# Kernel tuning notes

Hardware: AMD Instinct MI355X
Metric: run time of the kernel (lower is better)

## Reference

```python
import jax, jax.numpy as jnp
import numpy as np

N_NODES = 50000
N_EDGES = 800000
H = 128


def _mlp2(x, W1, b1, W2, b2):
    # Linear -> ReLU -> Linear
    h = jax.nn.relu(x @ W1 + b1)
    return h @ W2 + b2


def setup_inputs() -> dict:
    key = jax.random.key(0)
    ks = jax.random.split(key, 12)
    glorot = lambda k, fi, fo: jax.random.normal(k, (fi, fo), jnp.float32) * (1.0 / np.sqrt(fi))
    return {
        "x": jax.random.normal(ks[0], (N_NODES, H), jnp.float32),
        "edge_index": jax.random.randint(ks[1], (2, N_EDGES), 0, N_NODES, dtype=jnp.int64),
        "edge_attr": jax.random.normal(ks[2], (N_EDGES, H), jnp.float32),
        # edge MLP: 3H -> H -> H
        "We1": glorot(ks[3], 3 * H, H),
        "be1": jnp.zeros((H,), jnp.float32),
        "We2": glorot(ks[4], H, H),
        "be2": jnp.zeros((H,), jnp.float32),
        # node MLP: 2H -> H -> H
        "Wn1": glorot(ks[5], 2 * H, H),
        "bn1": jnp.zeros((H,), jnp.float32),
        "Wn2": glorot(ks[6], H, H),
        "bn2": jnp.zeros((H,), jnp.float32),
    }


def reference(x, edge_index, edge_attr, We1, be1, We2, be2, Wn1, bn1, Wn2, bn2):
    row, col = edge_index[0], edge_index[1]
    # gather + concat -> edge MLP  [E, 3H] -> [E, H]
    edge_inputs = jnp.concatenate([x[row], x[col], edge_attr], axis=-1)
    messages = _mlp2(edge_inputs, We1, be1, We2, be2)
    # scatter_add by destination node
    agg = jax.ops.segment_sum(messages, col, num_segments=x.shape[0])
    # concat -> node MLP  [N, 2H] -> [N, H]
    node_inputs = jnp.concatenate([x, agg], axis=-1)
    return _mlp2(node_inputs, Wn1, bn1, Wn2, bn2)
```

## Files before the change

### kernel.cpp

```cpp
#include <hip/hip_runtime.h>
#include <hip/hip_bf16.h>
#include <stdint.h>

#define N_NODES 50000
#define N_EDGES 800000
#define H 128

typedef short bf16x8 __attribute__((ext_vector_type(8)));
typedef float f32x4 __attribute__((ext_vector_type(4)));

__device__ __forceinline__ short f2bfs(float f) {
    __hip_bfloat16 h = __float2bfloat16(f);
    return *(short*)&h;
}

__device__ __forceinline__ bf16x8 cvt8(const float* __restrict__ p) {
    const float4* q = (const float4*)p;
    float4 a = q[0], b = q[1];
    bf16x8 r;
    r[0] = f2bfs(a.x); r[1] = f2bfs(a.y); r[2] = f2bfs(a.z); r[3] = f2bfs(a.w);
    r[4] = f2bfs(b.x); r[5] = f2bfs(b.y); r[6] = f2bfs(b.z); r[7] = f2bfs(b.w);
    return r;
}

__global__ void prep_weights(const float* __restrict__ We1, const float* __restrict__ We2,
                             const float* __restrict__ Wn1, const float* __restrict__ Wn2,
                             unsigned short* __restrict__ wb) {
    int i = blockIdx.x * 256 + threadIdx.x;
    if (i >= 114688) return;
    const float* W; int idx;
    if (i < 49152)      { W = We1; idx = i; }
    else if (i < 65536) { W = We2; idx = i - 49152; }
    else if (i < 98304) { W = Wn1; idx = i - 65536; }
    else                { W = Wn2; idx = i - 98304; }
    int f = idx >> 9, lane = (idx >> 3) & 63, j = idx & 7;
    int kt = f >> 3, nt = f & 7;
    int k = kt * 32 + (lane >> 4) * 8 + j;
    int n = nt * 16 + (lane & 15);
    wb[i] = (unsigned short)f2bfs(W[k * H + n]);
}

__launch_bounds__(256)
__global__ void edge_mlp(const float* __restrict__ x,
                         const int* __restrict__ ei,
                         const float* __restrict__ ea,
                         const float* __restrict__ be1,
                         const float* __restrict__ be2,
                         const unsigned short* __restrict__ wb,
                         float* __restrict__ agg) {
    __shared__ short hbuf[4][2][4][64][8];
    const int tid = threadIdx.x;
    const int wave = tid >> 6, lane = tid & 63;
    const int c = lane & 15, quad = lane >> 4;
    const int e0 = (blockIdx.x * 4 + wave) * 32;

    const bf16x8* __restrict__ BW1 = (const bf16x8*)wb;
    const bf16x8* __restrict__ BW2 = (const bf16x8*)(wb + 49152);

    float be1v[8], be2v[8];
#pragma unroll
    for (int nt = 0; nt < 8; ++nt) {
        be1v[nt] = be1[nt * 16 + c];
        be2v[nt] = be2[nt * 16 + c];
    }

    const float* pa[2][3];
#pragma unroll
    for (int t = 0; t < 2; ++t) {
        int e = e0 + t * 16 + c;
        int r  = ei[e];
        int cl = ei[N_EDGES + e];
        pa[t][0] = x + (size_t)r * H;
        pa[t][1] = x + (size_t)cl * H;
        pa[t][2] = ea + (size_t)e * H;
    }

    f32x4 acc[2][8];
#pragma unroll
    for (int t = 0; t < 2; ++t)
#pragma unroll
        for (int nt = 0; nt < 8; ++nt)
            acc[t][nt] = (f32x4){be1v[nt], be1v[nt], be1v[nt], be1v[nt]};

#pragma unroll
    for (int kt = 0; kt < 12; ++kt) {
        const int seg = kt >> 2;
        const int off = (kt & 3) * 32 + quad * 8;
        bf16x8 a0 = cvt8(pa[0][seg] + off);
        bf16x8 a1 = cvt8(pa[1][seg] + off);
#pragma unroll
        for (int nt = 0; nt < 8; ++nt) {
            bf16x8 b = BW1[(kt * 8 + nt) * 64 + lane];
            acc[0][nt] = __builtin_amdgcn_mfma_f32_16x16x32_bf16(a0, b, acc[0][nt], 0, 0, 0);
            acc[1][nt] = __builtin_amdgcn_mfma_f32_16x16x32_bf16(a1, b, acc[1][nt], 0, 0, 0);
        }
    }

#pragma unroll
    for (int t = 0; t < 2; ++t)
#pragma unroll
        for (int nt = 0; nt < 8; ++nt) {
            int kt2 = nt >> 1;
            int laneq = 16 * ((nt * 2 + (c >> 3)) & 3);
#pragma unroll
            for (int r = 0; r < 4; ++r) {
                float v = acc[t][nt][r];
                v = v > 0.f ? v : 0.f;
                hbuf[wave][t][kt2][quad * 4 + r + laneq][c & 7] = f2bfs(v);
            }
        }
    __syncthreads();

    f32x4 acc2[2][8];
#pragma unroll
    for (int t = 0; t < 2; ++t)
#pragma unroll
        for (int nt = 0; nt < 8; ++nt)
            acc2[t][nt] = (f32x4){be2v[nt], be2v[nt], be2v[nt], be2v[nt]};

#pragma unroll
    for (int kt = 0; kt < 4; ++kt) {
        bf16x8 a0 = *(const bf16x8*)&hbuf[wave][0][kt][lane][0];
        bf16x8 a1 = *(const bf16x8*)&hbuf[wave][1][kt][lane][0];
#pragma unroll
        for (int nt = 0; nt < 8; ++nt) {
            bf16x8 b = BW2[(kt * 8 + nt) * 64 + lane];
            acc2[0][nt] = __builtin_amdgcn_mfma_f32_16x16x32_bf16(a0, b, acc2[0][nt], 0, 0, 0);
            acc2[1][nt] = __builtin_amdgcn_mfma_f32_16x16x32_bf16(a1, b, acc2[1][nt], 0, 0, 0);
        }
    }

    int ce[2][4];
#pragma unroll
    for (int t = 0; t < 2; ++t)
#pragma unroll
        for (int r = 0; r < 4; ++r)
            ce[t][r] = ei[N_EDGES + e0 + t * 16 + quad * 4 + r];

#pragma unroll
    for (int t = 0; t < 2; ++t)
#pragma unroll
        for (int nt = 0; nt < 8; ++nt)
#pragma unroll
            for (int r = 0; r < 4; ++r)
                atomicAdd(agg + (size_t)ce[t][r] * H + nt * 16 + c, acc2[t][nt][r]);
}

__launch_bounds__(256)
__global__ void node_mlp(const float* __restrict__ x,
                         const float* __restrict__ agg,
                         const float* __restrict__ bn1,
                         const float* __restrict__ bn2,
                         const unsigned short* __restrict__ wb,
                         float* __restrict__ out) {
    __shared__ short hbuf[4][2][4][64][8];
    const int tid = threadIdx.x;
    const int wave = tid >> 6, lane = tid & 63;
    const int c = lane & 15, quad = lane >> 4;
    const int v0 = (blockIdx.x * 4 + wave) * 32;

    const bf16x8* __restrict__ BN1 = (const bf16x8*)(wb + 65536);
    const bf16x8* __restrict__ BN2 = (const bf16x8*)(wb + 98304);

    float b1v[8], b2v[8];
#pragma unroll
    for (int nt = 0; nt < 8; ++nt) {
        b1v[nt] = bn1[nt * 16 + c];
        b2v[nt] = bn2[nt * 16 + c];
    }

    const float* pa[2][2];
#pragma unroll
    for (int t = 0; t < 2; ++t) {
        int v = v0 + t * 16 + c;
        v = v < N_NODES ? v : N_NODES - 1;
        pa[t][0] = x   + (size_t)v * H;
        pa[t][1] = agg + (size_t)v * H;
    }

    f32x4 acc[2][8];
#pragma unroll
    for (int t = 0; t < 2; ++t)
#pragma unroll
        for (int nt = 0; nt < 8; ++nt)
            acc[t][nt] = (f32x4){b1v[nt], b1v[nt], b1v[nt], b1v[nt]};

#pragma unroll
    for (int kt = 0; kt < 8; ++kt) {
        const int seg = kt >> 2;
        const int off = (kt & 3) * 32 + quad * 8;
        bf16x8 a0 = cvt8(pa[0][seg] + off);
        bf16x8 a1 = cvt8(pa[1][seg] + off);
#pragma unroll
        for (int nt = 0; nt < 8; ++nt) {
            bf16x8 b = BN1[(kt * 8 + nt) * 64 + lane];
            acc[0][nt] = __builtin_amdgcn_mfma_f32_16x16x32_bf16(a0, b, acc[0][nt], 0, 0, 0);
            acc[1][nt] = __builtin_amdgcn_mfma_f32_16x16x32_bf16(a1, b, acc[1][nt], 0, 0, 0);
        }
    }

#pragma unroll
    for (int t = 0; t < 2; ++t)
#pragma unroll
        for (int nt = 0; nt < 8; ++nt) {
            int kt2 = nt >> 1;
            int laneq = 16 * ((nt * 2 + (c >> 3)) & 3);
#pragma unroll
            for (int r = 0; r < 4; ++r) {
                float v = acc[t][nt][r];
                v = v > 0.f ? v : 0.f;
                hbuf[wave][t][kt2][quad * 4 + r + laneq][c & 7] = f2bfs(v);
            }
        }
    __syncthreads();

    f32x4 acc2[2][8];
#pragma unroll
    for (int t = 0; t < 2; ++t)
#pragma unroll
        for (int nt = 0; nt < 8; ++nt)
            acc2[t][nt] = (f32x4){b2v[nt], b2v[nt], b2v[nt], b2v[nt]};

#pragma unroll
    for (int kt = 0; kt < 4; ++kt) {
        bf16x8 a0 = *(const bf16x8*)&hbuf[wave][0][kt][lane][0];
        bf16x8 a1 = *(const bf16x8*)&hbuf[wave][1][kt][lane][0];
#pragma unroll
        for (int nt = 0; nt < 8; ++nt) {
            bf16x8 b = BN2[(kt * 8 + nt) * 64 + lane];
            acc2[0][nt] = __builtin_amdgcn_mfma_f32_16x16x32_bf16(a0, b, acc2[0][nt], 0, 0, 0);
            acc2[1][nt] = __builtin_amdgcn_mfma_f32_16x16x32_bf16(a1, b, acc2[1][nt], 0, 0, 0);
        }
    }

#pragma unroll
    for (int t = 0; t < 2; ++t)
#pragma unroll
        for (int nt = 0; nt < 8; ++nt)
#pragma unroll
            for (int r = 0; r < 4; ++r) {
                int v = v0 + t * 16 + quad * 4 + r;
                if (v < N_NODES)
                    out[(size_t)v * H + nt * 16 + c] = acc2[t][nt][r];
            }
}

extern "C" void kernel_launch(void* const* d_in, const int* in_sizes, int n_in,
                              void* d_out, int out_size, void* d_ws, size_t ws_size,
                              hipStream_t stream) {
    const float* x   = (const float*)d_in[0];
    const int*   ei  = (const int*)d_in[1];
    const float* ea  = (const float*)d_in[2];
    const float* We1 = (const float*)d_in[3];
    const float* be1 = (const float*)d_in[4];
    const float* We2 = (const float*)d_in[5];
    const float* be2 = (const float*)d_in[6];
    const float* Wn1 = (const float*)d_in[7];
    const float* bn1 = (const float*)d_in[8];
    const float* Wn2 = (const float*)d_in[9];
    const float* bn2 = (const float*)d_in[10];
    float* out = (float*)d_out;

    unsigned short* wb = (unsigned short*)d_ws;
    float* agg = (float*)((char*)d_ws + (256 << 10));

    hipMemsetAsync(agg, 0, (size_t)N_NODES * H * sizeof(float), stream);
    prep_weights<<<448, 256, 0, stream>>>(We1, We2, Wn1, Wn2, wb);
    edge_mlp<<<6250, 256, 0, stream>>>(x, ei, ea, be1, be2, wb, agg);
    node_mlp<<<391, 256, 0, stream>>>(x, agg, bn1, bn2, wb, out);
}
```

Baseline: 1.033 ms.

## Sort edges by destination and pre-reduce messages before atomic scatter

Measured after the change: 1.215 ms. 1.18x slower.

```diff
diff --git a/kernel.cpp b/kernel.cpp
--- a/kernel.cpp
+++ b/kernel.cpp
@@ -40,20 +40,83 @@
     wb[i] = (unsigned short)f2bfs(W[k * H + n]);
 }
 
+__global__ void prep_x(const float* __restrict__ x, unsigned short* __restrict__ xb) {
+    int i = blockIdx.x * 256 + threadIdx.x;
+    if (i >= (N_NODES * H) / 8) return;
+    bf16x8 v = cvt8(x + (size_t)i * 8);
+    *(bf16x8*)(xb + (size_t)i * 8) = v;
+}
+
+__global__ void hist_col(const int* __restrict__ ei, int* __restrict__ cnt) {
+    int e = blockIdx.x * 256 + threadIdx.x;
+    if (e < N_EDGES) atomicAdd(&cnt[ei[N_EDGES + e]], 1);
+}
+
+__global__ void scan_hist(const int* __restrict__ cnt, int* __restrict__ cursor) {
+    __shared__ int wsum[16];
+    __shared__ int stot;
+    __shared__ int sbase_s;
+    const int tid = threadIdx.x;
+    const int lane = tid & 63, wid = tid >> 6;
+    if (tid == 0) sbase_s = 0;
+    __syncthreads();
+    for (int base = 0; base < N_NODES; base += 1024) {
+        int i = base + tid;
+        int v = (i < N_NODES) ? cnt[i] : 0;
+        int incl = v;
+#pragma unroll
+        for (int off = 1; off < 64; off <<= 1) {
+            int t = __shfl_up(incl, off);
+            if (lane >= off) incl += t;
+        }
+        if (lane == 63) wsum[wid] = incl;
+        __syncthreads();
+        if (wid == 0) {
+            int wv = (lane < 16) ? wsum[lane] : 0;
+            int winc = wv;
+#pragma unroll
+            for (int off = 1; off < 16; off <<= 1) {
+                int t = __shfl_up(winc, off);
+                if (lane >= off) winc += t;
+            }
+            if (lane < 16) wsum[lane] = winc - wv;
+            if (lane == 15) stot = winc;
+        }
+        __syncthreads();
+        if (i < N_NODES) cursor[i] = sbase_s + wsum[wid] + (incl - v);
+        __syncthreads();
+        if (tid == 0) sbase_s += stot;
+        __syncthreads();
+    }
+}
+
+__global__ void build_perm(const int* __restrict__ ei, int* __restrict__ cursor,
+                           int* __restrict__ perm) {
+    int e = blockIdx.x * 256 + threadIdx.x;
+    if (e < N_EDGES) {
+        int pos = atomicAdd(&cursor[ei[N_EDGES + e]], 1);
+        perm[pos] = e;
+    }
+}
+
 __launch_bounds__(256)
-__global__ void edge_mlp(const float* __restrict__ x,
+__global__ void edge_mlp(const unsigned short* __restrict__ xb,
                          const int* __restrict__ ei,
                          const float* __restrict__ ea,
                          const float* __restrict__ be1,
                          const float* __restrict__ be2,
                          const unsigned short* __restrict__ wb,
+                         const int* __restrict__ perm,
                          float* __restrict__ agg) {
-    __shared__ short hbuf[4][2][4][64][8];
+    __shared__ __align__(16) char smem[4][8192];
     const int tid = threadIdx.x;
     const int wave = tid >> 6, lane = tid & 63;
     const int c = lane & 15, quad = lane >> 4;
     const int e0 = (blockIdx.x * 4 + wave) * 32;
 
+    short (*hb)[4][64][8] = (short (*)[4][64][8])smem[wave];
+    float* msg = (float*)smem[wave];
+
     const bf16x8* __restrict__ BW1 = (const bf16x8*)wb;
     const bf16x8* __restrict__ BW2 = (const bf16x8*)(wb + 49152);
 
@@ -64,15 +127,19 @@
         be2v[nt] = be2[nt * 16 + c];
     }
 
-    const float* pa[2][3];
+    int myp = 0, myd = 0;
+    if (lane < 32) { myp = perm[e0 + lane]; myd = ei[N_EDGES + myp]; }
+
+    const unsigned short* pxb[2][2];
+    const float* pea[2];
 #pragma unroll
     for (int t = 0; t < 2; ++t) {
-        int e = e0 + t * 16 + c;
-        int r  = ei[e];
-        int cl = ei[N_EDGES + e];
-        pa[t][0] = x + (size_t)r * H;
-        pa[t][1] = x + (size_t)cl * H;
-        pa[t][2] = ea + (size_t)e * H;
+        int p_tc = __shfl(myp, t * 16 + c);
+        int d_tc = __shfl(myd, t * 16 + c);
+        int r_tc = ei[p_tc];
+        pxb[t][0] = xb + (size_t)r_tc * H;
+        pxb[t][1] = xb + (size_t)d_tc * H;
+        pea[t]    = ea + (size_t)p_tc * H;
     }
 
     f32x4 acc[2][8];
@@ -84,10 +151,15 @@
 
 #pragma unroll
     for (int kt = 0; kt < 12; ++kt) {
-        const int seg = kt >> 2;
         const int off = (kt & 3) * 32 + quad * 8;
-        bf16x8 a0 = cvt8(pa[0][seg] + off);
-        bf16x8 a1 = cvt8(pa[1][seg] + off);
+        bf16x8 a0, a1;
+        if (kt < 8) {
+            a0 = *(const bf16x8*)(pxb[0][kt >> 2] + off);
+            a1 = *(const bf16x8*)(pxb[1][kt >> 2] + off);
+        } else {
+            a0 = cvt8(pea[0] + off);
+            a1 = cvt8(pea[1] + off);
+        }
 #pragma unroll
         for (int nt = 0; nt < 8; ++nt) {
             bf16x8 b = BW1[(kt * 8 + nt) * 64 + lane];
@@ -106,7 +178,7 @@
             for (int r = 0; r < 4; ++r) {
                 float v = acc[t][nt][r];
                 v = v > 0.f ? v : 0.f;
-                hbuf[wave][t][kt2][quad * 4 + r + laneq][c & 7] = f2bfs(v);
+                hb[t][kt2][quad * 4 + r + laneq][c & 7] = f2bfs(v);
             }
         }
     __syncthreads();
@@ -120,8 +192,8 @@
 
 #pragma unroll
     for (int kt = 0; kt < 4; ++kt) {
-        bf16x8 a0 = *(const bf16x8*)&hbuf[wave][0][kt][lane][0];
-        bf16x8 a1 = *(const bf16x8*)&hbuf[wave][1][kt][lane][0];
+        bf16x8 a0 = *(const bf16x8*)&hb[0][kt][lane][0];
+        bf16x8 a1 = *(const bf16x8*)&hb[1][kt][lane][0];
 #pragma unroll
         for (int nt = 0; nt < 8; ++nt) {
             bf16x8 b = BW2[(kt * 8 + nt) * 64 + lane];
@@ -129,35 +201,52 @@
             acc2[1][nt] = __builtin_amdgcn_mfma_f32_16x16x32_bf16(a1, b, acc2[1][nt], 0, 0, 0);
         }
     }
-
-    int ce[2][4];
-#pragma unroll
-    for (int t = 0; t < 2; ++t)
-#pragma unroll
-        for (int r = 0; r < 4; ++r)
-            ce[t][r] = ei[N_EDGES + e0 + t * 16 + quad * 4 + r];
-
-#pragma unroll
-    for (int t = 0; t < 2; ++t)
+    __syncthreads();
+
+#pragma unroll
+    for (int t = 0; t < 2; ++t) {
 #pragma unroll
         for (int nt = 0; nt < 8; ++nt)
 #pragma unroll
             for (int r = 0; r < 4; ++r)
-                atomicAdd(agg + (size_t)ce[t][r] * H + nt * 16 + c, acc2[t][nt][r]);
-}
-
-__launch_bounds__(256)
-__global__ void node_mlp(const float* __restrict__ x,
+                msg[(quad * 4 + r) * 128 + ((nt * 16 + c) ^ (quad * 8))] = acc2[t][nt][r];
+        __syncthreads();
+
+        float s0 = 0.f, s1 = 0.f;
+        int dprev = __builtin_amdgcn_readlane(myd, t * 16);
+#pragma unroll
+        for (int i = 0; i < 16; ++i) {
+            int di = __builtin_amdgcn_readlane(myd, t * 16 + i);
+            int idx = i * 128 + (lane ^ ((i >> 2) * 8));
+            float v0 = msg[idx];
+            float v1 = msg[idx + 64];
+            if (i > 0 && di != dprev) {
+                atomicAdd(agg + (size_t)dprev * H + lane, s0);
+                atomicAdd(agg + (size_t)dprev * H + 64 + lane, s1);
+                s0 = v0; s1 = v1; dprev = di;
+            } else {
+                s0 += v0; s1 += v1;
+            }
+        }
+        atomicAdd(agg + (size_t)dprev * H + lane, s0);
+        atomicAdd(agg + (size_t)dprev * H + 64 + lane, s1);
+        __syncthreads();
+    }
+}
+
+__launch_bounds__(128)
+__global__ void node_mlp(const unsigned short* __restrict__ xb,
                          const float* __restrict__ agg,
                          const float* __restrict__ bn1,
                          const float* __restrict__ bn2,
                          const unsigned short* __restrict__ wb,
                          float* __restrict__ out) {
-    __shared__ short hbuf[4][2][4][64][8];
+    __shared__ __align__(16) char smem[2][8192];
     const int tid = threadIdx.x;
     const int wave = tid >> 6, lane = tid & 63;
     const int c = lane & 15, quad = lane >> 4;
-    const int v0 = (blockIdx.x * 4 + wave) * 32;
+    const int v0 = (blockIdx.x * 2 + wave) * 32;
+    short (*hb)[4][64][8] = (short (*)[4][64][8])smem[wave];
 
     const bf16x8* __restrict__ BN1 = (const bf16x8*)(wb + 65536);
     const bf16x8* __restrict__ BN2 = (const bf16x8*)(wb + 98304);
@@ -169,13 +258,14 @@
         b2v[nt] = bn2[nt * 16 + c];
     }
 
-    const float* pa[2][2];
+    const unsigned short* pxb[2];
+    const float* pag[2];
 #pragma unroll
     for (int t = 0; t < 2; ++t) {
         int v = v0 + t * 16 + c;
         v = v < N_NODES ? v : N_NODES - 1;
-        pa[t][0] = x   + (size_t)v * H;
-        pa[t][1] = agg + (size_t)v * H;
+        pxb[t] = xb  + (size_t)v * H;
+        pag[t] = agg + (size_t)v * H;
     }
 
     f32x4 acc[2][8];
@@ -187,10 +277,15 @@
 
 #pragma unroll
     for (int kt = 0; kt < 8; ++kt) {
-        const int seg = kt >> 2;
         const int off = (kt & 3) * 32 + quad * 8;
-        bf16x8 a0 = cvt8(pa[0][seg] + off);
-        bf16x8 a1 = cvt8(pa[1][seg] + off);
+        bf16x8 a0, a1;
+        if (kt < 4) {
+            a0 = *(const bf16x8*)(pxb[0] + off);
+            a1 = *(const bf16x8*)(pxb[1] + off);
+        } else {
+            a0 = cvt8(pag[0] + off);
+            a1 = cvt8(pag[1] + off);
+        }
 #pragma unroll
         for (int nt = 0; nt < 8; ++nt) {
             bf16x8 b = BN1[(kt * 8 + nt) * 64 + lane];
@@ -209,7 +304,7 @@
             for (int r = 0; r < 4; ++r) {
                 float v = acc[t][nt][r];
                 v = v > 0.f ? v : 0.f;
-                hbuf[wave][t][kt2][quad * 4 + r + laneq][c & 7] = f2bfs(v);
+                hb[t][kt2][quad * 4 + r + laneq][c & 7] = f2bfs(v);
             }
         }
     __syncthreads();
@@ -223,8 +318,8 @@
 
 #pragma unroll
     for (int kt = 0; kt < 4; ++kt) {
-        bf16x8 a0 = *(const bf16x8*)&hbuf[wave][0][kt][lane][0];
-        bf16x8 a1 = *(const bf16x8*)&hbuf[wave][1][kt][lane][0];
+        bf16x8 a0 = *(const bf16x8*)&hb[0][kt][lane][0];
+        bf16x8 a1 = *(const bf16x8*)&hb[1][kt][lane][0];
 #pragma unroll
         for (int nt = 0; nt < 8; ++nt) {
             bf16x8 b = BN2[(kt * 8 + nt) * 64 + lane];
@@ -261,11 +356,20 @@
     const float* bn2 = (const float*)d_in[10];
     float* out = (float*)d_out;
 
-    unsigned short* wb = (unsigned short*)d_ws;
-    float* agg = (float*)((char*)d_ws + (256 << 10));
-
-    hipMemsetAsync(agg, 0, (size_t)N_NODES * H * sizeof(float), stream);
+    char* base = (char*)d_ws;
+    unsigned short* wb   = (unsigned short*)base;
+    float*          agg  = (float*)(base + 262144);
+    int*            cnt  = (int*)(base + 25862144);
+    int*            cur  = (int*)(base + 26066944);
+    int*            perm = (int*)(base + 26271744);
+    unsigned short* xbuf = (unsigned short*)(base + 29471744);
+
+    hipMemsetAsync(agg, 0, 25600000 + 204800, stream);
     prep_weights<<<448, 256, 0, stream>>>(We1, We2, Wn1, Wn2, wb);
-    edge_mlp<<<6250, 256, 0, stream>>>(x, ei, ea, be1, be2, wb, agg);
-    node_mlp<<<391, 256, 0, stream>>>(x, agg, bn1, bn2, wb, out);
-}
+    prep_x<<<3125, 256, 0, stream>>>(x, xbuf);
+    hist_col<<<3125, 256, 0, stream>>>(ei, cnt);
+    scan_hist<<<1, 1024, 0, stream>>>(cnt, cur);
+    build_perm<<<3125, 256, 0, stream>>>(ei, cur, perm);
+    edge_mlp<<<6250, 256, 0, stream>>>(xbuf, ei, ea, be1, be2, wb, perm, agg);
+    node_mlp<<<782, 128, 0, stream>>>(xbuf, agg, bn1, bn2, wb, out);
+}
```
